# Optimization experiments

Measured on AMD Instinct MI355X. Metric: run time of the kernel, lower is better.

The kernel has to match this reference:

```python
import jax, jax.numpy as jnp
import numpy as np

B, S, T, D, H, HID, V, O = 8, 512, 256, 768, 12, 3072, 50257, 64
HD = D // H  # head dim = 64


def setup_inputs() -> dict:
    key = jax.random.key(0)
    ks = jax.random.split(key, 20)
    s = 0.02
    return {
        'source_input_ids': jax.random.randint(ks[0], (B, S), 0, V, dtype=jnp.int32),
        'encoder_hidden_states': jax.random.normal(ks[1], (B, S, D), dtype=jnp.float32),
        'encoder_attn_mask': jnp.zeros((B, S), dtype=bool),
        'decoder_hidden_states': jax.random.normal(ks[2], (B, T, D), dtype=jnp.float32),
        'onto_ids': jnp.arange(V - O, V, dtype=jnp.int32),
        # MultiheadAttention params (torch layout: W [out,in])
        'Wq': jax.random.normal(ks[3], (D, D)) * s, 'bq': jnp.zeros((D,)),
        'Wk': jax.random.normal(ks[4], (D, D)) * s, 'bk': jnp.zeros((D,)),
        'Wv': jax.random.normal(ks[5], (D, D)) * s, 'bv': jnp.zeros((D,)),
        'Wo': jax.random.normal(ks[6], (D, D)) * s, 'bo': jnp.zeros((D,)),
        # CopyHead: Linear(D, 1)
        'copy_w': jax.random.normal(ks[7], (D, 1)) * s, 'copy_b': jnp.zeros((1,)),
        # Generator FFN: Linear(D, HID) -> relu -> Linear(HID, O)
        'W1': jax.random.normal(ks[8], (HID, D)) * s, 'b1': jnp.zeros((HID,)),
        'W2': jax.random.normal(ks[9], (O, HID)) * s, 'b2': jnp.zeros((O,)),
    }


def _forward(source_input_ids, encoder_hidden_states, encoder_attn_mask,
             decoder_hidden_states, onto_ids, Wq, bq, Wk, bk, Wv, bv, Wo, bo,
             copy_w, copy_b, W1, b1, W2, b2):
    # ---- Generator: FFN + softmax over ontology vocab ----
    h = jax.nn.relu(decoder_hidden_states @ W1.T + b1)
    ontology_probs = jax.nn.softmax(h @ W2.T + b2, axis=-1)  # [B,T,O]

    # ---- MultiheadAttention (batch_first, eval: no dropout) ----
    q = (decoder_hidden_states @ Wq.T + bq).reshape(B, T, H, HD)
    k = (encoder_hidden_states @ Wk.T + bk).reshape(B, S, H, HD)
    v = (encoder_hidden_states @ Wv.T + bv).reshape(B, S, H, HD)
    scores = jnp.einsum('bthd,bshd->bhts', q, k) / jnp.sqrt(jnp.float32(HD))
    scores = jnp.where(encoder_attn_mask[:, None, None, :], -jnp.inf, scores)
    attn = jax.nn.softmax(scores, axis=-1)                       # [B,H,T,S]
    ctx = jnp.einsum('bhts,bshd->bthd', attn, v).reshape(B, T, D)
    context_outputs = ctx @ Wo.T + bo                            # [B,T,D]
    from_source_probs = attn.mean(axis=1)                        # avg heads [B,T,S]

    # ---- CopyHead ----
    copy_probs = jax.nn.sigmoid(context_outputs @ copy_w + copy_b)  # [B,T,1]

    from_source_probs = from_source_probs * copy_probs
    ontology_probs = ontology_probs * (1.0 - copy_probs)

    # ---- scatter-add into full vocab distribution ----
    bi = jnp.arange(B)[:, None, None]
    ti = jnp.arange(T)[None, :, None]
    vocab_probs = jnp.zeros((B, T, V), dtype=copy_probs.dtype)
    vocab_probs = vocab_probs.at[bi, ti, source_input_ids[:, None, :]].add(from_source_probs)
    vocab_probs = vocab_probs.at[bi, ti, onto_ids[None, None, :]].add(ontology_probs)
    return vocab_probs


def reference(source_input_ids, encoder_hidden_states, encoder_attn_mask,
              decoder_hidden_states, onto_ids, Wq, bq, Wk, bk, Wv, bv, Wo, bo,
              copy_w, copy_b, W1, b1, W2, b2):
    return _forward(source_input_ids, encoder_hidden_states, encoder_attn_mask,
                    decoder_hidden_states, onto_ids, Wq, bq, Wk, bk, Wv, bv,
                    Wo, bo, copy_w, copy_b, W1, b1, W2, b2)
```

## Files before the change

### kernel.cpp

```cpp
#include <hip/hip_runtime.h>
#include <hip/hip_bf16.h>
#include <math.h>

constexpr int B = 8, S = 512, T = 256, D = 768, H = 12, HID = 3072;
constexpr int V = 50257, O = 64, HD = 64;

typedef short bf16x8 __attribute__((ext_vector_type(8)));
typedef float f32x4 __attribute__((ext_vector_type(4)));

__device__ __forceinline__ float b2f(unsigned short u) {
  union { float f; unsigned v; } x; x.v = ((unsigned)u) << 16; return x.f;
}
__device__ __forceinline__ unsigned short f2b(float f) {
  __hip_bfloat16 h = __float2bfloat16(f);
  return *(unsigned short*)&h;
}

__device__ __forceinline__ void async16(const void* g, void* l) {
  __builtin_amdgcn_global_load_lds(
      (const __attribute__((address_space(1))) void*)g,
      (__attribute__((address_space(3))) void*)l, 16, 0, 0);
}

constexpr int CH0 = B * T * D / 8;
constexpr int CH1 = CH0 + B * S * D / 8;
constexpr int CH2 = CH1 + HID * D / 8;
constexpr int CH3 = CH2 + D * D / 8;
constexpr int CH4 = CH3 + D * D / 8;
constexpr int CH5 = CH4 + D * D / 8;
constexpr int CH6 = CH5 + O * HID / 8;

__global__ void cvt_weff_kernel(
    const float* __restrict__ dec, const float* __restrict__ enc,
    const float* __restrict__ W1, const float* __restrict__ Wq,
    const float* __restrict__ Wk, const float* __restrict__ Wv,
    const float* __restrict__ W2, const float* __restrict__ Wo,
    const float* __restrict__ bo, const float* __restrict__ cw,
    const float* __restrict__ cb,
    __hip_bfloat16* __restrict__ decb, __hip_bfloat16* __restrict__ encb,
    __hip_bfloat16* __restrict__ WA, __hip_bfloat16* __restrict__ WB,
    __hip_bfloat16* __restrict__ W2b, float* __restrict__ weff) {
  int i = blockIdx.x * blockDim.x + threadIdx.x;
  if (i >= CH6) {
    int j = i - CH6;
    if (j < D) {
      float acc = 0.f;
      for (int o = 0; o < D; ++o) acc += Wo[(size_t)o * D + j] * cw[o];
      weff[j] = acc;
    } else if (j == D) {
      float acc = cb[0];
      for (int o = 0; o < D; ++o) acc += bo[o] * cw[o];
      weff[D] = acc;
    }
    return;
  }
  const float* src;
  __hip_bfloat16* dst;
  int j;
  if (i < CH0)      { src = dec; dst = decb;                 j = i; }
  else if (i < CH1) { src = enc; dst = encb;                 j = i - CH0; }
  else if (i < CH2) { src = W1;  dst = WA;                   j = i - CH1; }
  else if (i < CH3) { src = Wq;  dst = WA + (size_t)HID * D; j = i - CH2; }
  else if (i < CH4) { src = Wk;  dst = WB;                   j = i - CH3; }
  else if (i < CH5) { src = Wv;  dst = WB + (size_t)D * D;   j = i - CH4; }
  else              { src = W2;  dst = W2b;                  j = i - CH5; }
  size_t e = (size_t)j * 8;
  float4 v0 = *(const float4*)&src[e];
  float4 v1 = *(const float4*)&src[e + 4];
  ushort4 o0, o1;
  o0.x = f2b(v0.x); o0.y = f2b(v0.y); o0.z = f2b(v0.z); o0.w = f2b(v0.w);
  o1.x = f2b(v1.x); o1.y = f2b(v1.y); o1.z = f2b(v1.z); o1.w = f2b(v1.w);
  *(ushort4*)&dst[e] = o0;
  *(ushort4*)&dst[e + 4] = o1;
}

template <int BN, int MODE>
__device__ __forceinline__ void gemm_body(
    const __hip_bfloat16* __restrict__ A, const __hip_bfloat16* __restrict__ W,
    const float* __restrict__ bias0, const float* __restrict__ bias1,
    float* __restrict__ Cf, __hip_bfloat16* __restrict__ out0,
    __hip_bfloat16* __restrict__ out1, int M, int N, int K,
    int bx, int by, int kbeg, int kend,
    __hip_bfloat16* Als, __hip_bfloat16* Bls) {
  constexpr int BK = 32;
  constexpr int WTN = BN / 2;
  constexpr int NFRAG = WTN / 16;
  const int tid = threadIdx.x;
  const int lane = tid & 63, wid = tid >> 6;
  const int wm = wid >> 1, wn = wid & 1;
  const int row0 = by * 128, col0 = bx * BN;
  const int lr = lane & 15;
  const int ko = (lane >> 4) * 8;

  f32x4 acc[4][NFRAG] = {};

  for (int k0 = kbeg; k0 < kend; k0 += BK) {
#pragma unroll
    for (int c = 0; c < 2; ++c) {
      int j = tid + c * 256;
      int r = j >> 2, col = (j & 3) * 8;
      async16(&A[(size_t)(row0 + r) * K + k0 + col], (void*)&Als[j * 8]);
    }
#pragma unroll
    for (int c = 0; c < BN / 64; ++c) {
      int j = tid + c * 256;
      int r = j >> 2, col = (j & 3) * 8;
      async16(&W[(size_t)(col0 + r) * K + k0 + col], (void*)&Bls[j * 8]);
    }
    __syncthreads();

    bf16x8 af[4], bfr[NFRAG];
#pragma unroll
    for (int mi = 0; mi < 4; ++mi)
      af[mi] = *(const bf16x8*)&Als[(wm * 64 + mi * 16 + lr) * BK + ko];
#pragma unroll
    for (int ni = 0; ni < NFRAG; ++ni)
      bfr[ni] = *(const bf16x8*)&Bls[(wn * WTN + ni * 16 + lr) * BK + ko];
#pragma unroll
    for (int mi = 0; mi < 4; ++mi)
#pragma unroll
      for (int ni = 0; ni < NFRAG; ++ni)
        acc[mi][ni] = __builtin_amdgcn_mfma_f32_16x16x32_bf16(
            af[mi], bfr[ni], acc[mi][ni], 0, 0, 0);
    __syncthreads();
  }

#pragma unroll
  for (int mi = 0; mi < 4; ++mi) {
    int rbase = row0 + wm * 64 + mi * 16 + (lane >> 4) * 4;
#pragma unroll
    for (int ni = 0; ni < NFRAG; ++ni) {
      int c = col0 + wn * WTN + ni * 16 + lr;
#pragma unroll
      for (int r = 0; r < 4; ++r) {
        int rr = rbase + r;
        float a = acc[mi][ni][r];
        if constexpr (MODE == 1) {
          if (c < HID) {
            out0[(size_t)rr * HID + c] = __float2bfloat16(fmaxf(a + bias0[c], 0.f));
          } else {
            out1[(size_t)rr * D + (c - HID)] = __float2bfloat16(a + bias1[c - HID]);
          }
        } else if constexpr (MODE == 2) {
          if (c < D) {
            out0[(size_t)rr * D + c] = __float2bfloat16(a + bias0[c]);
          } else {
            int d = c - D;
            size_t idx = (((size_t)(rr >> 9) * D + d) << 9) | (size_t)(rr & 511);
            out1[idx] = __float2bfloat16(a + bias1[d]);
          }
        } else {
          Cf[(size_t)rr * N + c] = a;
        }
      }
    }
  }
}

constexpr int KV_BX = (2 * D) / 128;
constexpr int KV_BLOCKS = KV_BX * (B * S / 128);
constexpr int FQ_BX = (HID + D) / 128;
constexpr int FQ_BLOCKS = FQ_BX * (B * T / 128);
constexpr int GEMM_BLOCKS = KV_BLOCKS + FQ_BLOCKS;
constexpr int ZERO_BLOCKS = 1184;
constexpr long long OUT_N4 = (long long)B * T * V / 4;

__global__ __launch_bounds__(256) void gemm_mega_kernel(
    const __hip_bfloat16* __restrict__ encb, const __hip_bfloat16* __restrict__ WB,
    const float* __restrict__ bk, const float* __restrict__ bv,
    __hip_bfloat16* __restrict__ kb16, __hip_bfloat16* __restrict__ vt,
    const __hip_bfloat16* __restrict__ decb, const __hip_bfloat16* __restrict__ WA,
    const float* __restrict__ b1, const float* __restrict__ bq,
    __hip_bfloat16* __restrict__ hb16, __hip_bfloat16* __restrict__ qb16,
    float* __restrict__ out) {
  __shared__ __hip_bfloat16 Als[128 * 32];
  __shared__ __hip_bfloat16 Bls[128 * 32];
  int bid = blockIdx.x;
  if (bid < KV_BLOCKS) {
    gemm_body<128, 2>(encb, WB, bk, bv, nullptr, kb16, vt,
                      B * S, 2 * D, D, bid % KV_BX, bid / KV_BX, 0, D, Als, Bls);
  } else if (bid < GEMM_BLOCKS) {
    int r = bid - KV_BLOCKS;
    gemm_body<128, 1>(decb, WA, b1, bq, nullptr, hb16, qb16,
                      B * T, HID + D, D, r % FQ_BX, r / FQ_BX, 0, D, Als, Bls);
  } else {
    long long zb = bid - GEMM_BLOCKS;
    f32x4* o4 = (f32x4*)out;
    const f32x4 z = {0.f, 0.f, 0.f, 0.f};
    for (long long i = zb * 256 + threadIdx.x; i < OUT_N4;
         i += (long long)ZERO_BLOCKS * 256)
      __builtin_nontemporal_store(z, &o4[i]);
  }
}

constexpr int NSPLIT = 16;
constexpr int KCH = HID / NSPLIT;

__global__ __launch_bounds__(256) void gemm_ffn2_kernel(
    const __hip_bfloat16* __restrict__ hb16, const __hip_bfloat16* __restrict__ W2b,
    float* __restrict__ part) {
  __shared__ __hip_bfloat16 Als[128 * 32];
  __shared__ __hip_bfloat16 Bls[64 * 32];
  int sp = blockIdx.x, mt = blockIdx.y;
  gemm_body<64, 3>(hb16, W2b, nullptr, nullptr,
                   part + (size_t)sp * (B * T) * 64, nullptr, nullptr,
                   B * T, 64, HID, 0, mt, sp * KCH, (sp + 1) * KCH, Als, Bls);
}

__global__ __launch_bounds__(256) void attention3_kernel(
    const __hip_bfloat16* __restrict__ q, const __hip_bfloat16* __restrict__ k,
    const __hip_bfloat16* __restrict__ vt, const unsigned char* __restrict__ mask,
    __hip_bfloat16* __restrict__ ctx, __hip_bfloat16* __restrict__ Pg) {
  constexpr int TB = 32;
  constexpr int SCP = 520;
  __shared__ __hip_bfloat16 Qls[TB * 64];
  __shared__ __hip_bfloat16 KVls[128 * 64];
  __shared__ __hip_bfloat16 sc[TB * SCP];
  const int tid = threadIdx.x;
  const int lane = tid & 63, w = tid >> 6;
  const int lr = lane & 15, lg = lane >> 4;
  const int bid = blockIdx.x;
  const int tile = bid & 7;
  const int h = (bid >> 3) % H;
  const int b = bid / (8 * H);
  const int t0 = tile * TB;

  {
    int r = tid >> 3, slot = tid & 7;
    int g = slot ^ (r & 7);
    async16(&q[((size_t)(b * T + t0 + r)) * D + h * 64 + g * 8],
            (void*)&Qls[tid * 8]);
  }

  for (int ch = 0; ch < 4; ++ch) {
    const int s0 = ch * 128;
#pragma unroll
    for (int it = 0; it < 4; ++it) {
      int c = tid + it * 256;
      int r = c >> 3, slot = c & 7;
      int g = slot ^ (r & 7);
      async16(&k[((size_t)(b * S + s0 + r)) * D + h * 64 + g * 8],
              (void*)&KVls[c * 8]);
    }
    __syncthreads();
    f32x4 acc[2][2] = {};
#pragma unroll
    for (int ks = 0; ks < 2; ++ks) {
      bf16x8 af[2], bfr[2];
#pragma unroll
      for (int mi = 0; mi < 2; ++mi) {
        int row = mi * 16 + lr;
        int slot = (4 * ks + lg) ^ (row & 7);
        af[mi] = *(const bf16x8*)&Qls[row * 64 + slot * 8];
      }
#pragma unroll
      for (int ni = 0; ni < 2; ++ni) {
        int row = w * 32 + ni * 16 + lr;
        int slot = (4 * ks + lg) ^ (row & 7);
        bfr[ni] = *(const bf16x8*)&KVls[row * 64 + slot * 8];
      }
#pragma unroll
      for (int mi = 0; mi < 2; ++mi)
#pragma unroll
        for (int ni = 0; ni < 2; ++ni)
          acc[mi][ni] = __builtin_amdgcn_mfma_f32_16x16x32_bf16(
              af[mi], bfr[ni], acc[mi][ni], 0, 0, 0);
    }
#pragma unroll
    for (int ni = 0; ni < 2; ++ni) {
      int s_local = w * 32 + ni * 16 + lr;
      bool msk = mask[b * S + s0 + s_local];
#pragma unroll
      for (int mi = 0; mi < 2; ++mi) {
        int trow = mi * 16 + lg * 4;
#pragma unroll
        for (int rg = 0; rg < 4; ++rg) {
          float val = msk ? -INFINITY : acc[mi][ni][rg] * 0.125f;
          sc[(trow + rg) * SCP + s0 + s_local] = __float2bfloat16(val);
        }
      }
    }
    __syncthreads();
  }

  unsigned short* scu = (unsigned short*)sc;
  unsigned short* pgu = (unsigned short*)Pg;
#pragma unroll
  for (int i = 0; i < 8; ++i) {
    int r = w * 8 + i;
    float x[8];
    float m = -INFINITY;
#pragma unroll
    for (int j = 0; j < 8; ++j) {
      x[j] = b2f(scu[r * SCP + j * 64 + lane]);
      m = fmaxf(m, x[j]);
    }
#pragma unroll
    for (int o = 32; o > 0; o >>= 1) m = fmaxf(m, __shfl_xor(m, o));
    float ssum = 0.f;
#pragma unroll
    for (int j = 0; j < 8; ++j) { x[j] = __expf(x[j] - m); ssum += x[j]; }
#pragma unroll
    for (int o = 32; o > 0; o >>= 1) ssum += __shfl_xor(ssum, o);
    float inv = 1.f / ssum;
#pragma unroll
    for (int j = 0; j < 8; ++j) {
      unsigned short pb = f2b(x[j] * inv);
      scu[r * SCP + j * 64 + lane] = pb;
      pgu[(((size_t)(b * H + h)) * T + t0 + r) * S + j * 64 + lane] = pb;
    }
  }
  __syncthreads();

  f32x4 accp[2] = {};
  for (int ch = 0; ch < 4; ++ch) {
    const int s0 = ch * 128;
#pragma unroll
    for (int it = 0; it < 4; ++it) {
      int c = tid + it * 256;
      int d = c >> 4, slot = c & 15;
      int g = slot ^ (d & 7);
      async16(&vt[(((size_t)(b * H + h)) * 64 + d) * S + s0 + g * 8],
              (void*)&KVls[c * 8]);
    }
    __syncthreads();
#pragma unroll
    for (int ks = 0; ks < 4; ++ks) {
      bf16x8 bfr;
      {
        int brow = w * 16 + lr;
        int slot = (4 * ks + lg) ^ (brow & 7);
        bfr = *(const bf16x8*)&KVls[brow * 128 + slot * 8];
      }
#pragma unroll
      for (int mi = 0; mi < 2; ++mi) {
        int prow = mi * 16 + lr;
        bf16x8 af = *(const bf16x8*)&sc[prow * SCP + s0 + ks * 32 + lg * 8];
        accp[mi] = __builtin_amdgcn_mfma_f32_16x16x32_bf16(af, bfr, accp[mi], 0, 0, 0);
      }
    }
    __syncthreads();
  }
#pragma unroll
  for (int mi = 0; mi < 2; ++mi) {
    int trow = mi * 16 + lg * 4;
#pragma unroll
    for (int rg = 0; rg < 4; ++rg) {
      ctx[((size_t)(b * T + t0 + trow + rg)) * D + h * 64 + w * 16 + lr] =
          __float2bfloat16(accp[mi][rg]);
    }
  }
}

__global__ __launch_bounds__(256) void scatter3_kernel(
    const int* __restrict__ src, const int* __restrict__ onto,
    const __hip_bfloat16* __restrict__ Pg, const float* __restrict__ part,
    const float* __restrict__ b2v, const __hip_bfloat16* __restrict__ ctx,
    const float* __restrict__ weff, float* __restrict__ out) {
  const int bt = blockIdx.x;
  const int b = bt >> 8, t = bt & (T - 1);
  const int tid = threadIdx.x;
  const int lane = tid & 63;
  float* row = out + (size_t)bt * V;

  __shared__ float red[256];
  __shared__ float onts[O];

  const unsigned short* cu = (const unsigned short*)ctx + (size_t)bt * D;
  float a = 0.f;
#pragma unroll
  for (int j = 0; j < 3; ++j) {
    int d = j * 256 + tid;
    a += b2f(cu[d]) * weff[d];
  }
  red[tid] = a;
  __syncthreads();
  for (int st = 128; st > 0; st >>= 1) {
    if (tid < st) red[tid] += red[tid + st];
    __syncthreads();
  }
  const float cpv = 1.f / (1.f + __expf(-(red[0] + weff[D])));
  __syncthreads();

  if (tid < 64) {
    float x = b2v[lane];
#pragma unroll
    for (int sp = 0; sp < NSPLIT; ++sp)
      x += part[((size_t)sp * (B * T) + bt) * 64 + lane];
    float m = x;
#pragma unroll
    for (int o = 32; o > 0; o >>= 1) m = fmaxf(m, __shfl_xor(m, o));
    float e = __expf(x - m);
    float ss = e;
#pragma unroll
    for (int o = 32; o > 0; o >>= 1) ss += __shfl_xor(ss, o);
    onts[lane] = e / ss * (1.f - cpv);
  }
  __syncthreads();

  const unsigned short* pg = (const unsigned short*)Pg;
#pragma unroll
  for (int jj = 0; jj < 2; ++jj) {
    int s = jj * 256 + tid;
    float sum = 0.f;
#pragma unroll
    for (int h = 0; h < H; ++h)
      sum += b2f(pg[(((size_t)(b * H + h)) * T + t) * S + s]);
    atomicAdd(&row[src[b * S + s]], sum * (1.0f / (float)H) * cpv);
  }
  if (tid < O) atomicAdd(&row[onto[tid]], onts[tid]);
}

extern "C" void kernel_launch(void* const* d_in, const int* in_sizes, int n_in,
                              void* d_out, int out_size, void* d_ws, size_t ws_size,
                              hipStream_t stream) {
  const int* src_ids = (const int*)d_in[0];
  const float* enc = (const float*)d_in[1];
  const unsigned char* mask = (const unsigned char*)d_in[2];
  const float* dec = (const float*)d_in[3];
  const int* onto_ids = (const int*)d_in[4];
  const float* Wq = (const float*)d_in[5];
  const float* bq = (const float*)d_in[6];
  const float* Wk = (const float*)d_in[7];
  const float* bk = (const float*)d_in[8];
  const float* Wv = (const float*)d_in[9];
  const float* bv = (const float*)d_in[10];
  const float* Wo = (const float*)d_in[11];
  const float* bo = (const float*)d_in[12];
  const float* copy_w = (const float*)d_in[13];
  const float* copy_b = (const float*)d_in[14];
  const float* W1 = (const float*)d_in[15];
  const float* b1 = (const float*)d_in[16];
  const float* W2 = (const float*)d_in[17];
  const float* b2 = (const float*)d_in[18];

  const int MT = B * T;
  const int MS = B * S;

  __hip_bfloat16* wb = (__hip_bfloat16*)d_ws;
  __hip_bfloat16* qb16 = wb;    wb += (size_t)MT * D;
  __hip_bfloat16* kb16 = wb;    wb += (size_t)MS * D;
  __hip_bfloat16* vt = wb;      wb += (size_t)MS * D;
  __hip_bfloat16* ctxb16 = wb;  wb += (size_t)MT * D;
  __hip_bfloat16* W2b = wb;     wb += (size_t)O * HID;
  __hip_bfloat16* WB = wb;      wb += (size_t)2 * D * D;
  __hip_bfloat16* WA = wb;      wb += (size_t)(HID + D) * D;
  __hip_bfloat16* Pg = wb;
  __hip_bfloat16* decb = wb;
  __hip_bfloat16* encb = decb + (size_t)MT * D;
  __hip_bfloat16* hb16 = encb + (size_t)MS * D;
  wb += (size_t)B * H * T * S;
  float* wf = (float*)wb;
  float* part = wf;             wf += (size_t)NSPLIT * MT * O;
  float* weff = wf;             wf += (size_t)(D + 1);

  float* out = (float*)d_out;

  cvt_weff_kernel<<<CH6 / 256 + 4, 256, 0, stream>>>(
      dec, enc, W1, Wq, Wk, Wv, W2, Wo, bo, copy_w, copy_b,
      decb, encb, WA, WB, W2b, weff);

  gemm_mega_kernel<<<GEMM_BLOCKS + ZERO_BLOCKS, 256, 0, stream>>>(
      encb, WB, bk, bv, kb16, vt, decb, WA, b1, bq, hb16, qb16, out);

  gemm_ffn2_kernel<<<dim3(NSPLIT, MT / 128), 256, 0, stream>>>(hb16, W2b, part);

  attention3_kernel<<<B * H * (T / 32), 256, 0, stream>>>(
      qb16, kb16, vt, mask, ctxb16, Pg);

  scatter3_kernel<<<MT, 256, 0, stream>>>(
      src_ids, onto_ids, Pg, part, b2, ctxb16, weff, out);
}
```

Before: 281.8 us.

## Merge attention and FFN2 into one launch and split output zeroing across kernels

Fuses the FFN2 split-K GEMM and the attention kernel into a single launch that dispatches on block index and shares one dynamically carved shared-memory buffer. The zero-fill of the large output buffer is split in half, with one half done in the first GEMM kernel and the other half in the fused attention kernel, so the bandwidth-bound stores overlap with compute in both launches. hb16 is moved to its own workspace region, since it can no longer alias the Pg buffer that attention now writes concurrently. This removes one kernel launch boundary, at the cost of a larger uniform LDS allocation for FFN2 blocks, which may reduce their occupancy.

```diff
diff --git a/kernel.cpp b/kernel.cpp
--- a/kernel.cpp
+++ b/kernel.cpp
@@ -74,6 +74,18 @@
   *(ushort4*)&dst[e + 4] = o1;
 }
 
+__device__ __forceinline__ void zero_range(float* out, long long lo4,
+                                           long long hi4, int zb, int nzb) {
+  f32x4* o4 = (f32x4*)out;
+  const f32x4 z = {0.f, 0.f, 0.f, 0.f};
+  for (long long i = lo4 + (long long)zb * 256 + threadIdx.x; i < hi4;
+       i += (long long)nzb * 256)
+    __builtin_nontemporal_store(z, &o4[i]);
+}
+
+constexpr long long OUT_N4 = (long long)B * T * V / 4;
+constexpr long long HALF4 = OUT_N4 / 2;
+
 template <int BN, int MODE>
 __device__ __forceinline__ void gemm_body(
     const __hip_bfloat16* __restrict__ A, const __hip_bfloat16* __restrict__ W,
@@ -162,8 +174,7 @@
 constexpr int FQ_BX = (HID + D) / 128;
 constexpr int FQ_BLOCKS = FQ_BX * (B * T / 128);
 constexpr int GEMM_BLOCKS = KV_BLOCKS + FQ_BLOCKS;
-constexpr int ZERO_BLOCKS = 1184;
-constexpr long long OUT_N4 = (long long)B * T * V / 4;
+constexpr int Z1 = 1024;
 
 __global__ __launch_bounds__(256) void gemm_mega_kernel(
     const __hip_bfloat16* __restrict__ encb, const __hip_bfloat16* __restrict__ WB,
@@ -184,42 +195,30 @@
     gemm_body<128, 1>(decb, WA, b1, bq, nullptr, hb16, qb16,
                       B * T, HID + D, D, r % FQ_BX, r / FQ_BX, 0, D, Als, Bls);
   } else {
-    long long zb = bid - GEMM_BLOCKS;
-    f32x4* o4 = (f32x4*)out;
-    const f32x4 z = {0.f, 0.f, 0.f, 0.f};
-    for (long long i = zb * 256 + threadIdx.x; i < OUT_N4;
-         i += (long long)ZERO_BLOCKS * 256)
-      __builtin_nontemporal_store(z, &o4[i]);
+    zero_range(out, 0, HALF4, bid - GEMM_BLOCKS, Z1);
   }
 }
 
 constexpr int NSPLIT = 16;
 constexpr int KCH = HID / NSPLIT;
-
-__global__ __launch_bounds__(256) void gemm_ffn2_kernel(
-    const __hip_bfloat16* __restrict__ hb16, const __hip_bfloat16* __restrict__ W2b,
-    float* __restrict__ part) {
-  __shared__ __hip_bfloat16 Als[128 * 32];
-  __shared__ __hip_bfloat16 Bls[64 * 32];
-  int sp = blockIdx.x, mt = blockIdx.y;
-  gemm_body<64, 3>(hb16, W2b, nullptr, nullptr,
-                   part + (size_t)sp * (B * T) * 64, nullptr, nullptr,
-                   B * T, 64, HID, 0, mt, sp * KCH, (sp + 1) * KCH, Als, Bls);
-}
-
-__global__ __launch_bounds__(256) void attention3_kernel(
+constexpr int FFN2_BLOCKS = NSPLIT * (B * T / 128);
+
+constexpr int ATTN_BLOCKS = B * H * (T / 32);
+constexpr int Z2 = 1024;
+
+__device__ void attn_body(
     const __hip_bfloat16* __restrict__ q, const __hip_bfloat16* __restrict__ k,
     const __hip_bfloat16* __restrict__ vt, const unsigned char* __restrict__ mask,
-    __hip_bfloat16* __restrict__ ctx, __hip_bfloat16* __restrict__ Pg) {
+    __hip_bfloat16* __restrict__ ctx, __hip_bfloat16* __restrict__ Pg,
+    int bid, char* smem) {
   constexpr int TB = 32;
   constexpr int SCP = 520;
-  __shared__ __hip_bfloat16 Qls[TB * 64];
-  __shared__ __hip_bfloat16 KVls[128 * 64];
-  __shared__ __hip_bfloat16 sc[TB * SCP];
+  __hip_bfloat16* Qls = (__hip_bfloat16*)smem;
+  __hip_bfloat16* KVls = Qls + TB * 64;
+  __hip_bfloat16* sc = KVls + 128 * 64;
   const int tid = threadIdx.x;
   const int lane = tid & 63, w = tid >> 6;
   const int lr = lane & 15, lg = lane >> 4;
-  const int bid = blockIdx.x;
   const int tile = bid & 7;
   const int h = (bid >> 3) % H;
   const int b = bid / (8 * H);
@@ -349,6 +348,29 @@
       ctx[((size_t)(b * T + t0 + trow + rg)) * D + h * 64 + w * 16 + lr] =
           __float2bfloat16(accp[mi][rg]);
     }
+  }
+}
+
+__global__ __launch_bounds__(256) void attn_ffn2_kernel(
+    const __hip_bfloat16* __restrict__ q, const __hip_bfloat16* __restrict__ k,
+    const __hip_bfloat16* __restrict__ vt, const unsigned char* __restrict__ mask,
+    __hip_bfloat16* __restrict__ ctx, __hip_bfloat16* __restrict__ Pg,
+    const __hip_bfloat16* __restrict__ hb16, const __hip_bfloat16* __restrict__ W2b,
+    float* __restrict__ part, float* __restrict__ out) {
+  __shared__ __align__(16) char smem[53760];
+  int bid = blockIdx.x;
+  if (bid < ATTN_BLOCKS) {
+    attn_body(q, k, vt, mask, ctx, Pg, bid, smem);
+  } else if (bid < ATTN_BLOCKS + FFN2_BLOCKS) {
+    int r = bid - ATTN_BLOCKS;
+    int sp = r & (NSPLIT - 1), mt = r / NSPLIT;
+    __hip_bfloat16* Als = (__hip_bfloat16*)smem;
+    __hip_bfloat16* Bls = Als + 128 * 32;
+    gemm_body<64, 3>(hb16, W2b, nullptr, nullptr,
+                     part + (size_t)sp * (B * T) * 64, nullptr, nullptr,
+                     B * T, 64, HID, 0, mt, sp * KCH, (sp + 1) * KCH, Als, Bls);
+  } else {
+    zero_range(out, HALF4, OUT_N4, bid - ATTN_BLOCKS - FFN2_BLOCKS, Z2);
   }
 }
 
@@ -445,10 +467,10 @@
   __hip_bfloat16* W2b = wb;     wb += (size_t)O * HID;
   __hip_bfloat16* WB = wb;      wb += (size_t)2 * D * D;
   __hip_bfloat16* WA = wb;      wb += (size_t)(HID + D) * D;
+  __hip_bfloat16* hb16 = wb;    wb += (size_t)MT * HID;
   __hip_bfloat16* Pg = wb;
   __hip_bfloat16* decb = wb;
   __hip_bfloat16* encb = decb + (size_t)MT * D;
-  __hip_bfloat16* hb16 = encb + (size_t)MS * D;
   wb += (size_t)B * H * T * S;
   float* wf = (float*)wb;
   float* part = wf;             wf += (size_t)NSPLIT * MT * O;
@@ -460,13 +482,11 @@
       dec, enc, W1, Wq, Wk, Wv, W2, Wo, bo, copy_w, copy_b,
       decb, encb, WA, WB, W2b, weff);
 
-  gemm_mega_kernel<<<GEMM_BLOCKS + ZERO_BLOCKS, 256, 0, stream>>>(
+  gemm_mega_kernel<<<GEMM_BLOCKS + Z1, 256, 0, stream>>>(
       encb, WB, bk, bv, kb16, vt, decb, WA, b1, bq, hb16, qb16, out);
 
-  gemm_ffn2_kernel<<<dim3(NSPLIT, MT / 128), 256, 0, stream>>>(hb16, W2b, part);
-
-  attention3_kernel<<<B * H * (T / 32), 256, 0, stream>>>(
-      qb16, kb16, vt, mask, ctxb16, Pg);
+  attn_ffn2_kernel<<<ATTN_BLOCKS + FFN2_BLOCKS + Z2, 256, 0, stream>>>(
+      qb16, kb16, vt, mask, ctxb16, Pg, hb16, W2b, part, out);
 
   scatter3_kernel<<<MT, 256, 0, stream>>>(
       src_ids, onto_ids, Pg, part, b2, ctxb16, weff, out);
```

New measurement: 282.7 us. Within noise of the previous version (+0.3%).
